# Kernel tuning notes

Measured on AMD Instinct MI355X. Metric: run time of the kernel, lower is better.

## Reference

```python
import jax, jax.numpy as jnp
import numpy as np

N_NODES = 50000
N_EDGES = 600000
CHANNELS = 128
HEADS = 8


def setup_inputs() -> dict:
    key = jax.random.key(0)
    k1, k2, k3 = jax.random.split(key, 3)
    x = jax.random.normal(k1, (N_NODES, CHANNELS), dtype=jnp.float32)
    edge_index = jax.random.randint(k2, (2, N_EDGES), 0, N_NODES, dtype=jnp.int32)
    att = jax.random.normal(k3, (HEADS, 2 * (CHANNELS // HEADS)), dtype=jnp.float32)
    return {"x": x, "edge_index": edge_index, "att": att}


def reference(x, edge_index, att):
    # x: [N, C], edge_index: [2, E], att: [H, 2*D] with D = C // H
    src, dst = edge_index[0], edge_index[1]
    n = x.shape[0]
    h = att.shape[0]
    d = att.shape[1] // 2

    x_src = x[src].reshape(-1, h, d)   # [E, H, D]
    x_dst = x[dst].reshape(-1, h, d)   # [E, H, D]

    # (cat([x_src, x_dst]) * att).sum(-1) == x_src @ att[:, :D] + x_dst @ att[:, D:]
    a_src, a_dst = att[:, :d], att[:, d:]
    alpha = jnp.einsum('ehd,hd->eh', x_src, a_src) + jnp.einsum('ehd,hd->eh', x_dst, a_dst)
    alpha = jnp.where(alpha >= 0, alpha, 0.2 * alpha)  # LeakyReLU(0.2)

    # segment softmax over dst; torch scatter_reduce amax includes the zero init,
    # so the per-node max is max(segment_max, 0)
    seg_max = jax.ops.segment_max(alpha, dst, num_segments=n)  # [N, H]
    seg_max = jnp.maximum(seg_max, 0.0)
    alpha = jnp.exp(alpha - seg_max[dst])
    seg_sum = jax.ops.segment_sum(alpha, dst, num_segments=n)  # [N, H]
    alpha = alpha / jnp.maximum(seg_sum[dst], 1e-10)

    # weighted scatter-add of source features
    weighted = x_src * alpha[..., None]                        # [E, H, D]
    out = jax.ops.segment_sum(weighted, dst, num_segments=n)   # [N, H, D]
    return out.reshape(n, -1)
```

## Files before the change

kernel.cpp:

```cpp
#include <hip/hip_runtime.h>

#define N_NODES  50000
#define N_EDGES  600000
#define CHANNELS 128
#define HEADS    8
#define HEAD_DIM 16
#define CAP      64

#define NBINS    256
#define CHUNK_E  1024
#define NCHUNK   ((N_EDGES + CHUNK_E - 1) / CHUNK_E)
#define SEGCAP   2816
#define NPB      200

#define LOGIT_VB ((N_NODES * (CHANNELS / 8)) / 256)
#define WPB      4

__device__ __forceinline__ unsigned bf16rne(float f) {
    unsigned u = __float_as_uint(f);
    return (u + 0x7FFFu + ((u >> 16) & 1u)) >> 16;
}

__global__ void hist_logit_kernel(const float* __restrict__ x,
                                  const float* __restrict__ att,
                                  const int*   __restrict__ dst,
                                  int*            __restrict__ hist,
                                  float*          __restrict__ ls8,
                                  float*          __restrict__ ld8,
                                  unsigned short* __restrict__ xb) {
    int b = blockIdx.x;
    int t = threadIdx.x;
    if (b < NCHUNK) {
        __shared__ int lh[NBINS];
        lh[t] = 0;
        __syncthreads();
        int base = b * CHUNK_E;
#pragma unroll
        for (int k = 0; k < 4; ++k) {
            int e = base + t + k * 256;
            if (e < N_EDGES) {
                unsigned bin = (unsigned)(dst[e] * NBINS) / N_NODES;
                atomicAdd(&lh[bin], 1);
            }
        }
        __syncthreads();
        hist[t * NCHUNK + b] = lh[t];
    } else {
        int gid = (b - NCHUNK) * 256 + t;
        int n  = gid >> 4;
        int c8 = gid & 15;
        int h  = c8 >> 1;
        int j8 = c8 & 1;

        const float4* xp = (const float4*)x + (size_t)gid * 2;
        float4 v0 = xp[0], v1 = xp[1];

        uint4 pk;
        pk.x = bf16rne(v0.x) | (bf16rne(v0.y) << 16);
        pk.y = bf16rne(v0.z) | (bf16rne(v0.w) << 16);
        pk.z = bf16rne(v1.x) | (bf16rne(v1.y) << 16);
        pk.w = bf16rne(v1.z) | (bf16rne(v1.w) << 16);
        ((uint4*)xb)[gid] = pk;

        const float4* att4 = (const float4*)att;
        float4 as0 = att4[h * 8 + j8 * 2],     as1 = att4[h * 8 + j8 * 2 + 1];
        float4 ad0 = att4[h * 8 + 4 + j8 * 2], ad1 = att4[h * 8 + 5 + j8 * 2];
        float ts = v0.x*as0.x + v0.y*as0.y + v0.z*as0.z + v0.w*as0.w
                 + v1.x*as1.x + v1.y*as1.y + v1.z*as1.z + v1.w*as1.w;
        float td = v0.x*ad0.x + v0.y*ad0.y + v0.z*ad0.z + v0.w*ad0.w
                 + v1.x*ad1.x + v1.y*ad1.y + v1.z*ad1.z + v1.w*ad1.w;
        ts += __shfl_xor(ts, 1, 2);
        td += __shfl_xor(td, 1, 2);
        if (j8 == 0) {
            ls8[n * HEADS + h] = ts;
            ld8[n * HEADS + h] = td;
        }
    }
}

__global__ void scan_kernel(const int* __restrict__ hist,
                            int* __restrict__ offm,
                            int* __restrict__ bincnt) {
    __shared__ int lds[256];
    int bin = blockIdx.x;
    int t = threadIdx.x;
    int c0 = t, c1 = t + 256, c2 = t + 512;
    int v0 = hist[bin * NCHUNK + c0];
    int v1 = (c1 < NCHUNK) ? hist[bin * NCHUNK + c1] : 0;
    int v2 = (c2 < NCHUNK) ? hist[bin * NCHUNK + c2] : 0;
    int s = v0 + v1 + v2;
    lds[t] = s;
    __syncthreads();
    for (int off = 1; off < 256; off <<= 1) {
        int u = (t >= off) ? lds[t - off] : 0;
        __syncthreads();
        lds[t] += u;
        __syncthreads();
    }
    int base = lds[t] - s;
    offm[c0 * NBINS + bin] = base;
    if (c1 < NCHUNK) offm[c1 * NBINS + bin] = base + v0;
    if (c2 < NCHUNK) offm[c2 * NBINS + bin] = base + v0 + v1;
    if (t == 255) bincnt[bin] = lds[255];
}

__global__ void binscatter_kernel(const int* __restrict__ src,
                                  const int* __restrict__ dst,
                                  const int* __restrict__ offm,
                                  unsigned*  __restrict__ ebuf) {
    __shared__ int loff[NBINS];
    __shared__ int lcnt[NBINS];
    int b = blockIdx.x;
    int t = threadIdx.x;
    loff[t] = offm[b * NBINS + t];
    lcnt[t] = 0;
    __syncthreads();
    int base = b * CHUNK_E;
#pragma unroll
    for (int k = 0; k < 4; ++k) {
        int e = base + t + k * 256;
        if (e < N_EDGES) {
            int d = dst[e];
            int s = src[e];
            unsigned bin = (unsigned)(d * NBINS) / N_NODES;
            int r = atomicAdd(&lcnt[bin], 1) + loff[bin];
            if (r < SEGCAP)
                ebuf[(size_t)bin * SEGCAP + r] = (unsigned)s | ((unsigned)d << 16);
        }
    }
}

__global__ void bucket_kernel(const unsigned* __restrict__ ebuf,
                              const int*      __restrict__ bincnt,
                              int*            __restrict__ cursor,
                              unsigned short* __restrict__ bucket) {
    __shared__ unsigned short rows[NPB * CAP];
    __shared__ int lcnt[NPB];
    int b = blockIdx.x;
    int t = threadIdx.x;
    int n0 = (b * N_NODES + NBINS - 1) / NBINS;
    int n1 = ((b + 1) * N_NODES + NBINS - 1) / NBINS;
    int nn = n1 - n0;
    if (t < NPB) lcnt[t] = 0;
    __syncthreads();
    int cnt = min(bincnt[b], SEGCAP);
    for (int i = t; i < cnt; i += 256) {
        unsigned rec = ebuf[(size_t)b * SEGCAP + i];
        int s = (int)(rec & 0xFFFFu);
        int d = (int)(rec >> 16);
        int pos = atomicAdd(&lcnt[d - n0], 1);
        if (pos < CAP) rows[(d - n0) * CAP + pos] = (unsigned short)s;
    }
    __syncthreads();
    int nq = nn * (CAP * 2 / 16);
    uint4* gdst = (uint4*)(bucket + (size_t)n0 * CAP);
    const uint4* lsrc = (const uint4*)rows;
    for (int i = t; i < nq; i += 256) gdst[i] = lsrc[i];
    if (t < nn) cursor[n0 + t] = lcnt[t];
}

__global__ void fused_gat_kernel(const unsigned short* __restrict__ xb,
                                 const float* __restrict__ ls8,
                                 const float* __restrict__ ld8,
                                 const int*   __restrict__ cursor,
                                 const unsigned short* __restrict__ bucket,
                                 float*       __restrict__ out) {
    __shared__ float s_p[WPB * CAP * HEADS];

    int wave = threadIdx.x >> 6;
    int lane = threadIdx.x & 63;
    int n = blockIdx.x * WPB + wave;
    if (n >= N_NODES) return;
    int h = lane >> 3;
    int j = lane & 7;
    int r   = lane >> 5;
    int l32 = lane & 31;
    int h2  = l32 >> 2;

    int   cnt_raw = cursor[n];
    int   myidx   = (int)bucket[(size_t)n * CAP + lane];
    float ldst    = ld8[n * HEADS + h];
    int cnt = (cnt_raw > CAP) ? CAP : cnt_raw;

    float* sp = s_p + wave * (CAP * HEADS);

    float av[8];
    float mymax = -1e30f;
#pragma unroll
    for (int k = 0; k < 8; ++k) {
        int i = j + 8 * k;
        av[k] = -1e30f;
        if (i < cnt) {
            int   s  = __shfl(myidx, i);
            float lg = ls8[s * HEADS + h] + ldst;
            float a  = (lg >= 0.0f) ? lg : 0.2f * lg;
            av[k] = a;
            mymax = fmaxf(mymax, a);
        }
    }
#pragma unroll
    for (int o = 4; o >= 1; o >>= 1) mymax = fmaxf(mymax, __shfl_xor(mymax, o, 8));
    float m = fmaxf(mymax, 0.0f);

    float myl = 0.0f;
#pragma unroll
    for (int k = 0; k < 8; ++k) {
        int i = j + 8 * k;
        if (i < cnt) {
            float p = __expf(av[k] - m);
            sp[i * HEADS + h] = p;
            myl += p;
        }
    }
#pragma unroll
    for (int o = 4; o >= 1; o >>= 1) myl += __shfl_xor(myl, o, 8);

#define LP(k) ( ((const uint2*)(xb + (size_t)__shfl(myidx, ((2*(k)+r) < cnt) ? (2*(k)+r) : 0) * CHANNELS))[l32] )
    uint2 q[8];
#pragma unroll
    for (int k = 0; k < 8; ++k) q[k] = LP(k);

    float a0 = 0.f, a1 = 0.f, a2 = 0.f, a3 = 0.f;
    int npair = (cnt + 1) >> 1;
    int k = 0;
    for (; k + 4 <= npair; k += 4) {
#pragma unroll
        for (int u = 0; u < 4; ++u) {
            int e2 = 2 * (k + u) + r;
            float p = (e2 < cnt) ? sp[e2 * HEADS + h2] : 0.0f;
            uint2 qq = q[u];
            a0 += p * __uint_as_float(qq.x << 16);
            a1 += p * __uint_as_float(qq.x & 0xFFFF0000u);
            a2 += p * __uint_as_float(qq.y << 16);
            a3 += p * __uint_as_float(qq.y & 0xFFFF0000u);
        }
#pragma unroll
        for (int u = 0; u < 4; ++u) q[u] = q[u + 4];
#pragma unroll
        for (int u = 0; u < 4; ++u) q[u + 4] = LP(k + 8 + u);
    }
    for (; k < npair; ++k) {
        int e2 = 2 * k + r;
        float p = (e2 < cnt) ? sp[e2 * HEADS + h2] : 0.0f;
        uint2 qq = q[0];
        a0 += p * __uint_as_float(qq.x << 16);
        a1 += p * __uint_as_float(qq.x & 0xFFFF0000u);
        a2 += p * __uint_as_float(qq.y << 16);
        a3 += p * __uint_as_float(qq.y & 0xFFFF0000u);
#pragma unroll
        for (int u = 0; u < 7; ++u) q[u] = q[u + 1];
    }
#undef LP

    a0 += __shfl_xor(a0, 32);
    a1 += __shfl_xor(a1, 32);
    a2 += __shfl_xor(a2, 32);
    a3 += __shfl_xor(a3, 32);

    float denom = __shfl(myl, h2 * 8);
    float inv = 1.0f / fmaxf(denom, 1e-10f);

    if (lane < 32) {
        float4 o4 = make_float4(a0 * inv, a1 * inv, a2 * inv, a3 * inv);
        ((float4*)(out + (size_t)n * CHANNELS))[l32] = o4;
    }
}

extern "C" void kernel_launch(void* const* d_in, const int* in_sizes, int n_in,
                              void* d_out, int out_size, void* d_ws, size_t ws_size,
                              hipStream_t stream) {
    const float* x   = (const float*)d_in[0];
    const int*   ei  = (const int*)  d_in[1];
    const float* att = (const float*)d_in[2];
    const int* src = ei;
    const int* dst = ei + N_EDGES;
    float* out = (float*)d_out;

    int*            hist   = (int*)d_ws;
    int*            offm   = hist + (size_t)NBINS * NCHUNK;
    int*            bincnt = offm + (size_t)NCHUNK * NBINS;
    unsigned*       ebuf   = (unsigned*)(bincnt + NBINS);
    int*            cursor = (int*)(ebuf + (size_t)NBINS * SEGCAP);
    unsigned short* bucket = (unsigned short*)(cursor + N_NODES);
    float*          ls8    = (float*)(bucket + (size_t)N_NODES * CAP);
    float*          ld8    = ls8 + (size_t)N_NODES * HEADS;
    unsigned short* xb     = (unsigned short*)(ld8 + (size_t)N_NODES * HEADS);

    hist_logit_kernel<<<NCHUNK + LOGIT_VB, 256, 0, stream>>>(
        x, att, dst, hist, ls8, ld8, xb);
    scan_kernel<<<NBINS, 256, 0, stream>>>(hist, offm, bincnt);
    binscatter_kernel<<<NCHUNK, 256, 0, stream>>>(src, dst, offm, ebuf);
    bucket_kernel<<<NBINS, 256, 0, stream>>>(ebuf, bincnt, cursor, bucket);
    fused_gat_kernel<<<(N_NODES + WPB - 1) / WPB, 64 * WPB, 0, stream>>>(
        xb, ls8, ld8, cursor, bucket, out);
}
```

Measured before the change: 138.1 us.

## Replace binned counting-sort CSR build with direct global-atomic bucket scatter

Drops the histogram, scan, bin-scatter and LDS bucketing kernels and builds the per-node source buckets with one global atomicAdd per edge on a per-node cursor. The cursor is zeroed inside the feature-prep kernel, so the pipeline shrinks from five launches to three. This removes launch overhead and the intermediate edge buffer traffic, but adds 600k contended global atomics and scattered 2-byte writes into the bucket array. Edge order inside each bucket becomes nondeterministic, which changes the floating-point summation order.

Result: slower. 161.4 us (+16.8%).

```diff
diff --git a/kernel.cpp b/kernel.cpp
--- a/kernel.cpp
+++ b/kernel.cpp
@@ -7,11 +7,8 @@
 #define HEAD_DIM 16
 #define CAP      64
 
-#define NBINS    256
 #define CHUNK_E  1024
 #define NCHUNK   ((N_EDGES + CHUNK_E - 1) / CHUNK_E)
-#define SEGCAP   2816
-#define NPB      200
 
 #define LOGIT_VB ((N_NODES * (CHANNELS / 8)) / 256)
 #define WPB      4
@@ -21,142 +18,62 @@
     return (u + 0x7FFFu + ((u >> 16) & 1u)) >> 16;
 }
 
-__global__ void hist_logit_kernel(const float* __restrict__ x,
-                                  const float* __restrict__ att,
-                                  const int*   __restrict__ dst,
-                                  int*            __restrict__ hist,
-                                  float*          __restrict__ ls8,
-                                  float*          __restrict__ ld8,
-                                  unsigned short* __restrict__ xb) {
-    int b = blockIdx.x;
+__global__ void xprep_kernel(const float* __restrict__ x,
+                             const float* __restrict__ att,
+                             float*          __restrict__ ls8,
+                             float*          __restrict__ ld8,
+                             unsigned short* __restrict__ xb,
+                             int*            __restrict__ cursor) {
+    int gid = blockIdx.x * 256 + threadIdx.x;
+    if (gid < N_NODES) cursor[gid] = 0;
+
+    int n  = gid >> 4;
+    int c8 = gid & 15;
+    int h  = c8 >> 1;
+    int j8 = c8 & 1;
+
+    const float4* xp = (const float4*)x + (size_t)gid * 2;
+    float4 v0 = xp[0], v1 = xp[1];
+
+    uint4 pk;
+    pk.x = bf16rne(v0.x) | (bf16rne(v0.y) << 16);
+    pk.y = bf16rne(v0.z) | (bf16rne(v0.w) << 16);
+    pk.z = bf16rne(v1.x) | (bf16rne(v1.y) << 16);
+    pk.w = bf16rne(v1.z) | (bf16rne(v1.w) << 16);
+    ((uint4*)xb)[gid] = pk;
+
+    const float4* att4 = (const float4*)att;
+    float4 as0 = att4[h * 8 + j8 * 2],     as1 = att4[h * 8 + j8 * 2 + 1];
+    float4 ad0 = att4[h * 8 + 4 + j8 * 2], ad1 = att4[h * 8 + 5 + j8 * 2];
+    float ts = v0.x*as0.x + v0.y*as0.y + v0.z*as0.z + v0.w*as0.w
+             + v1.x*as1.x + v1.y*as1.y + v1.z*as1.z + v1.w*as1.w;
+    float td = v0.x*ad0.x + v0.y*ad0.y + v0.z*ad0.z + v0.w*ad0.w
+             + v1.x*ad1.x + v1.y*ad1.y + v1.z*ad1.z + v1.w*ad1.w;
+    ts += __shfl_xor(ts, 1, 2);
+    td += __shfl_xor(td, 1, 2);
+    if (j8 == 0) {
+        ls8[n * HEADS + h] = ts;
+        ld8[n * HEADS + h] = td;
+    }
+}
+
+__global__ void scatter_kernel(const int* __restrict__ src,
+                               const int* __restrict__ dst,
+                               int*            __restrict__ cursor,
+                               unsigned short* __restrict__ bucket) {
+    int base = blockIdx.x * CHUNK_E;
     int t = threadIdx.x;
-    if (b < NCHUNK) {
-        __shared__ int lh[NBINS];
-        lh[t] = 0;
-        __syncthreads();
-        int base = b * CHUNK_E;
-#pragma unroll
-        for (int k = 0; k < 4; ++k) {
-            int e = base + t + k * 256;
-            if (e < N_EDGES) {
-                unsigned bin = (unsigned)(dst[e] * NBINS) / N_NODES;
-                atomicAdd(&lh[bin], 1);
-            }
-        }
-        __syncthreads();
-        hist[t * NCHUNK + b] = lh[t];
-    } else {
-        int gid = (b - NCHUNK) * 256 + t;
-        int n  = gid >> 4;
-        int c8 = gid & 15;
-        int h  = c8 >> 1;
-        int j8 = c8 & 1;
-
-        const float4* xp = (const float4*)x + (size_t)gid * 2;
-        float4 v0 = xp[0], v1 = xp[1];
-
-        uint4 pk;
-        pk.x = bf16rne(v0.x) | (bf16rne(v0.y) << 16);
-        pk.y = bf16rne(v0.z) | (bf16rne(v0.w) << 16);
-        pk.z = bf16rne(v1.x) | (bf16rne(v1.y) << 16);
-        pk.w = bf16rne(v1.z) | (bf16rne(v1.w) << 16);
-        ((uint4*)xb)[gid] = pk;
-
-        const float4* att4 = (const float4*)att;
-        float4 as0 = att4[h * 8 + j8 * 2],     as1 = att4[h * 8 + j8 * 2 + 1];
-        float4 ad0 = att4[h * 8 + 4 + j8 * 2], ad1 = att4[h * 8 + 5 + j8 * 2];
-        float ts = v0.x*as0.x + v0.y*as0.y + v0.z*as0.z + v0.w*as0.w
-                 + v1.x*as1.x + v1.y*as1.y + v1.z*as1.z + v1.w*as1.w;
-        float td = v0.x*ad0.x + v0.y*ad0.y + v0.z*ad0.z + v0.w*ad0.w
-                 + v1.x*ad1.x + v1.y*ad1.y + v1.z*ad1.z + v1.w*ad1.w;
-        ts += __shfl_xor(ts, 1, 2);
-        td += __shfl_xor(td, 1, 2);
-        if (j8 == 0) {
-            ls8[n * HEADS + h] = ts;
-            ld8[n * HEADS + h] = td;
-        }
-    }
-}
-
-__global__ void scan_kernel(const int* __restrict__ hist,
-                            int* __restrict__ offm,
-                            int* __restrict__ bincnt) {
-    __shared__ int lds[256];
-    int bin = blockIdx.x;
-    int t = threadIdx.x;
-    int c0 = t, c1 = t + 256, c2 = t + 512;
-    int v0 = hist[bin * NCHUNK + c0];
-    int v1 = (c1 < NCHUNK) ? hist[bin * NCHUNK + c1] : 0;
-    int v2 = (c2 < NCHUNK) ? hist[bin * NCHUNK + c2] : 0;
-    int s = v0 + v1 + v2;
-    lds[t] = s;
-    __syncthreads();
-    for (int off = 1; off < 256; off <<= 1) {
-        int u = (t >= off) ? lds[t - off] : 0;
-        __syncthreads();
-        lds[t] += u;
-        __syncthreads();
-    }
-    int base = lds[t] - s;
-    offm[c0 * NBINS + bin] = base;
-    if (c1 < NCHUNK) offm[c1 * NBINS + bin] = base + v0;
-    if (c2 < NCHUNK) offm[c2 * NBINS + bin] = base + v0 + v1;
-    if (t == 255) bincnt[bin] = lds[255];
-}
-
-__global__ void binscatter_kernel(const int* __restrict__ src,
-                                  const int* __restrict__ dst,
-                                  const int* __restrict__ offm,
-                                  unsigned*  __restrict__ ebuf) {
-    __shared__ int loff[NBINS];
-    __shared__ int lcnt[NBINS];
-    int b = blockIdx.x;
-    int t = threadIdx.x;
-    loff[t] = offm[b * NBINS + t];
-    lcnt[t] = 0;
-    __syncthreads();
-    int base = b * CHUNK_E;
 #pragma unroll
     for (int k = 0; k < 4; ++k) {
         int e = base + t + k * 256;
         if (e < N_EDGES) {
             int d = dst[e];
             int s = src[e];
-            unsigned bin = (unsigned)(d * NBINS) / N_NODES;
-            int r = atomicAdd(&lcnt[bin], 1) + loff[bin];
-            if (r < SEGCAP)
-                ebuf[(size_t)bin * SEGCAP + r] = (unsigned)s | ((unsigned)d << 16);
-        }
-    }
-}
-
-__global__ void bucket_kernel(const unsigned* __restrict__ ebuf,
-                              const int*      __restrict__ bincnt,
-                              int*            __restrict__ cursor,
-                              unsigned short* __restrict__ bucket) {
-    __shared__ unsigned short rows[NPB * CAP];
-    __shared__ int lcnt[NPB];
-    int b = blockIdx.x;
-    int t = threadIdx.x;
-    int n0 = (b * N_NODES + NBINS - 1) / NBINS;
-    int n1 = ((b + 1) * N_NODES + NBINS - 1) / NBINS;
-    int nn = n1 - n0;
-    if (t < NPB) lcnt[t] = 0;
-    __syncthreads();
-    int cnt = min(bincnt[b], SEGCAP);
-    for (int i = t; i < cnt; i += 256) {
-        unsigned rec = ebuf[(size_t)b * SEGCAP + i];
-        int s = (int)(rec & 0xFFFFu);
-        int d = (int)(rec >> 16);
-        int pos = atomicAdd(&lcnt[d - n0], 1);
-        if (pos < CAP) rows[(d - n0) * CAP + pos] = (unsigned short)s;
-    }
-    __syncthreads();
-    int nq = nn * (CAP * 2 / 16);
-    uint4* gdst = (uint4*)(bucket + (size_t)n0 * CAP);
-    const uint4* lsrc = (const uint4*)rows;
-    for (int i = t; i < nq; i += 256) gdst[i] = lsrc[i];
-    if (t < nn) cursor[n0 + t] = lcnt[t];
+            int pos = atomicAdd(&cursor[d], 1);
+            if (pos < CAP)
+                bucket[(size_t)d * CAP + pos] = (unsigned short)s;
+        }
+    }
 }
 
 __global__ void fused_gat_kernel(const unsigned short* __restrict__ xb,
@@ -276,21 +193,14 @@
     const int* dst = ei + N_EDGES;
     float* out = (float*)d_out;
 
-    int*            hist   = (int*)d_ws;
-    int*            offm   = hist + (size_t)NBINS * NCHUNK;
-    int*            bincnt = offm + (size_t)NCHUNK * NBINS;
-    unsigned*       ebuf   = (unsigned*)(bincnt + NBINS);
-    int*            cursor = (int*)(ebuf + (size_t)NBINS * SEGCAP);
+    int*            cursor = (int*)d_ws;
     unsigned short* bucket = (unsigned short*)(cursor + N_NODES);
     float*          ls8    = (float*)(bucket + (size_t)N_NODES * CAP);
     float*          ld8    = ls8 + (size_t)N_NODES * HEADS;
     unsigned short* xb     = (unsigned short*)(ld8 + (size_t)N_NODES * HEADS);
 
-    hist_logit_kernel<<<NCHUNK + LOGIT_VB, 256, 0, stream>>>(
-        x, att, dst, hist, ls8, ld8, xb);
-    scan_kernel<<<NBINS, 256, 0, stream>>>(hist, offm, bincnt);
-    binscatter_kernel<<<NCHUNK, 256, 0, stream>>>(src, dst, offm, ebuf);
-    bucket_kernel<<<NBINS, 256, 0, stream>>>(ebuf, bincnt, cursor, bucket);
+    xprep_kernel<<<LOGIT_VB, 256, 0, stream>>>(x, att, ls8, ld8, xb, cursor);
+    scatter_kernel<<<NCHUNK, 256, 0, stream>>>(src, dst, cursor, bucket);
     fused_gat_kernel<<<(N_NODES + WPB - 1) / WPB, 64 * WPB, 0, stream>>>(
         xb, ls8, ld8, cursor, bucket, out);
 }
```
